# Optimization experiments

Measured on AMD Instinct MI355X. Metric: run time of the kernel, lower is better.

## Reference

```python
import jax, jax.numpy as jnp
import numpy as np

SLOPE = 0.01  # torch LeakyReLU default negative_slope

def _leaky(v):
    return jnp.where(v >= 0, v, SLOPE * v)

def _conv3d(x, w, b, stride):
    y = jax.lax.conv_general_dilated(
        x, w, window_strides=(stride, stride, stride), padding='VALID',
        dimension_numbers=('NCDHW', 'OIDHW', 'NCDHW'))
    return y + b[None, :, None, None, None]

def setup_inputs() -> dict:
    key = jax.random.key(0)
    ks = jax.random.split(key, 12)
    s = 0.05  # small init scale to keep exp(L1) numerically sane
    x = jax.random.normal(ks[0], (64, 1, 92, 92, 92), dtype=jnp.float32)
    w1 = jax.random.normal(ks[1], (16, 1, 6, 6, 6), dtype=jnp.float32) * s
    b1 = jnp.zeros((16,), jnp.float32)
    w2 = jax.random.normal(ks[2], (32, 16, 5, 5, 5), dtype=jnp.float32) * s
    b2 = jnp.zeros((32,), jnp.float32)
    w3 = jax.random.normal(ks[3], (48, 32, 5, 5, 5), dtype=jnp.float32) * s
    b3 = jnp.zeros((48,), jnp.float32)
    w4 = jax.random.normal(ks[4], (64, 48, 3, 3, 3), dtype=jnp.float32) * s
    b4 = jnp.zeros((64,), jnp.float32)
    T = jax.random.normal(ks[5], (512, 64 * 16), dtype=jnp.float32) * s
    Wm = jax.random.normal(ks[6], (512 + 64, 1), dtype=jnp.float32) * s
    bm = jnp.zeros((1,), jnp.float32)
    return {'x': x, 'w1': w1, 'b1': b1, 'w2': w2, 'b2': b2, 'w3': w3,
            'b3': b3, 'w4': w4, 'b4': b4, 'T': T, 'Wm': Wm, 'bm': bm}

def reference(x, w1, b1, w2, b2, w3, b3, w4, b4, T, Wm, bm):
    h = _leaky(_conv3d(x, w1, b1, 2))   # [N,16,44,44,44]
    h = _leaky(_conv3d(h, w2, b2, 3))   # [N,32,14,14,14]
    h = _leaky(_conv3d(h, w3, b3, 3))   # [N,48,4,4,4]
    h = _leaky(_conv3d(h, w4, b4, 1))   # [N,64,2,2,2]
    feature = h.reshape(h.shape[0], -1)  # [N,512]
    # minibatch discrimination: M [N,64,16]
    M = (feature @ T).reshape(-1, 64, 16)
    # pairwise L1 over last dim -> [N,N,64]; sum_j exp(.) -> [N,64]
    dist = jnp.sum(jnp.abs(M[:, None, :, :] - M[None, :, :, :]), axis=-1)
    out_T = jnp.sum(jnp.exp(dist), axis=1)
    z = jnp.concatenate([feature, out_T], axis=1) @ Wm + bm
    return jax.nn.sigmoid(z)
```

## Files before the change

### kernel.cpp

```cpp
#include <hip/hip_runtime.h>
#include <hip/hip_bf16.h>
#include <hip/hip_fp16.h>

typedef _Float16 v2h __attribute__((ext_vector_type(2)));
typedef _Float16 v8h __attribute__((ext_vector_type(8)));
typedef __fp16  v2hf __attribute__((ext_vector_type(2)));
typedef float v4f __attribute__((ext_vector_type(4)));

static inline __device__ float leaky(float v) { return v >= 0.f ? v : 0.01f * v; }

static inline __device__ v2h pkrtz(float a, float b) {
    v2hf r = __builtin_amdgcn_cvt_pkrtz(a, b);
    return __builtin_bit_cast(v2h, r);
}

#define W4T_OFF   0
#define H3P_OFF   82944
#define H3_OFF    1655808
#define FEAT_OFF  1852416
#define M_OFF     1885184
#define OT_OFF    1950720
#define F16_BASE  1954816
#define WL1_OFF   0
#define BF2_OFF   4608
#define BF3_OFF   81408
#define H2C_OFF   273408
#define H1C_OFF   5893120

__global__ void prep_kernel(const float* __restrict__ w1, const float* __restrict__ w2,
                            const float* __restrict__ w3, const float* __restrict__ w4,
                            float* __restrict__ w4t, _Float16* __restrict__ Bw1,
                            _Float16* __restrict__ Bf2, _Float16* __restrict__ Bf3) {
    int i = blockIdx.x * 256 + threadIdx.x;
    if (i < 4608) {
        int ks = i >> 9, l = (i >> 3) & 63, j = i & 7;
        int oc = l & 15, kg = l >> 4;
        int g = ks * 4 + kg;
        int kz = g / 6, ky = g % 6;
        Bw1[i] = (j < 6) ? (_Float16)w1[oc * 216 + kz * 36 + ky * 6 + j]
                         : (_Float16)0.f;
    } else if (i < 4608 + 76800) {
        int j2 = i - 4608;
        int nt = j2 / 38400, r = j2 % 38400;
        int t = r / 512, l = (r % 512) >> 3, j = r & 7;
        int oc = nt * 16 + (l & 15);
        int k = (l >> 4) * 8 + j;
        int kz = t / 15, ky = (t % 15) / 3, kxp = t % 3;
        int kx = kxp * 2 + (k >= 16 ? 1 : 0);
        int ic = k & 15;
        Bf2[j2] = (kx < 5) ? (_Float16)w2[oc * 2000 + ic * 125 + kz * 25 + ky * 5 + kx]
                           : (_Float16)0.f;
    } else if (i < 4608 + 76800 + 192000) {
        int j3 = i - (4608 + 76800);
        int nt = j3 / 64000, r = j3 % 64000;
        int tap = r / 512, l = (r % 512) >> 3, j = r & 7;
        int oc = nt * 16 + (l & 15);
        int ic = (l >> 4) * 8 + j;
        Bf3[j3] = (_Float16)w3[oc * 4000 + ic * 125 + tap];
    } else {
        int j4 = i - (4608 + 76800 + 192000);
        if (j4 < 82944) {
            int oc = j4 & 63, t = j4 >> 6;
            w4t[j4] = w4[oc * 1296 + t];
        }
    }
}

__global__ __launch_bounds__(256) void conv1_kernel(
    const float* __restrict__ x, const _Float16* __restrict__ Bw1,
    const float* __restrict__ b1, _Float16* __restrict__ h1c, int n0) {
    __shared__ __align__(16) _Float16 tile[144 * 96];
    int tid = threadIdx.x;
    int b = blockIdx.x;
    int nb = b / 121, rr = b % 121;
    int zq = rr / 11, yt = rr % 11;
    const float* xin = x + (long)(n0 + nb) * 778688;
    int izb = 8 * zq, iyb = 8 * yt;

    for (int u = tid; u < 3312; u += 256) {
        int row = u / 23, c = u % 23;
        int iz = izb + row / 12, iy = iyb + row % 12;
        const float4 v = *(const float4*)(xin + (long)iz * 8464 + iy * 92 + 4 * c);
        union { v2h h[2]; uint2 u2; } pk;
        pk.h[0] = pkrtz(v.x, v.y);
        pk.h[1] = pkrtz(v.z, v.w);
        *(uint2*)(tile + row * 96 + 4 * c) = pk.u2;
    }
    if (tid < 144) {
        uint2 zz; zz.x = 0u; zz.y = 0u;
        *(uint2*)(tile + tid * 96 + 92) = zz;
    }
    __syncthreads();

    int lane = tid & 63, wv = tid >> 6;
    int col = lane & 15, kg = lane >> 4;

    v8h Bv[9];
#pragma unroll
    for (int ks = 0; ks < 9; ks++) Bv[ks] = *(const v8h*)(Bw1 + ks * 512 + lane * 8);

    int offs[9];
#pragma unroll
    for (int ks = 0; ks < 9; ks++) {
        int g = ks * 4 + kg;
        int kz = g / 6, ky = g % 6;
        offs[ks] = (kz * 12 + ky) * 192;
    }
    float bias = b1[col];
    const uint* lds32 = (const uint*)tile;

    int z = zq * 4 + wv;
    for (int yy = 0; yy < 4; yy++) {
#pragma unroll
        for (int xt = 0; xt < 3; xt++) {
            int xo_base = (xt == 2) ? 28 : (xt << 4);
            int base_byte = (24 * wv + 2 * yy) * 192 + (xo_base + col) * 4;
            v4f acc = {0.f, 0.f, 0.f, 0.f};
#pragma unroll
            for (int ks = 0; ks < 9; ks++) {
                int di = (base_byte + offs[ks]) >> 2;
                union { uint u[4]; v8h h; } A;
                A.u[0] = lds32[di + 0];
                A.u[1] = lds32[di + 1];
                A.u[2] = lds32[di + 2];
                A.u[3] = lds32[di + 3];
                acc = __builtin_amdgcn_mfma_f32_16x16x32_f16(A.h, Bv[ks], acc, 0, 0, 0);
            }
            int y = yt * 4 + yy;
            long obase = ((long)((nb * 44 + z) * 44 + y) * 44 + xo_base + kg * 4) * 16 + col;
#pragma unroll
            for (int reg = 0; reg < 4; reg++) {
                h1c[obase + reg * 16] = (_Float16)leaky(acc[reg] + bias);
            }
        }
    }
}

__global__ __launch_bounds__(256) void conv2_kernel(
    const _Float16* __restrict__ h1c, const _Float16* __restrict__ Bf2,
    const float* __restrict__ b2, _Float16* __restrict__ h2c, int n0, int mlimit) {
    int tid = threadIdx.x;
    int lane = tid & 63, wv = tid >> 6;
    int t0 = (blockIdx.x * 4 + wv) * 2;
    int col = lane & 15, kgrp = lane >> 4;
    int par = kgrp >> 1, ico = (kgrp & 1) * 8;

    int base[2];
    bool valid[2];
#pragma unroll
    for (int i = 0; i < 2; i++) {
        int m = (t0 + i) * 16 + col;
        valid[i] = m < mlimit;
        int mm = valid[i] ? m : 0;
        int nl = mm / 2744, r = mm % 2744;
        int z = r / 196; r %= 196;
        int y = r / 14, xx = r % 14;
        base[i] = nl * 1362944 + z * 3 * 30976 + y * 3 * 704 + xx * 3 * 16 + ico + par * 16;
    }

    v4f acc[2][2];
#pragma unroll
    for (int i = 0; i < 2; i++)
#pragma unroll
        for (int nt = 0; nt < 2; nt++) acc[i][nt] = (v4f){0.f, 0.f, 0.f, 0.f};

    int t = 0;
    for (int kz = 0; kz < 5; kz++) {
        for (int ky = 0; ky < 5; ky++) {
#pragma unroll
            for (int kxp = 0; kxp < 3; kxp++, t++) {
                int d = kz * 30976 + ky * 704 + kxp * 32;
                v8h A0 = *(const v8h*)(h1c + base[0] + d);
                v8h A1 = *(const v8h*)(h1c + base[1] + d);
                v8h B0 = *(const v8h*)(Bf2 + t * 512 + lane * 8);
                v8h B1 = *(const v8h*)(Bf2 + (75 + t) * 512 + lane * 8);
                acc[0][0] = __builtin_amdgcn_mfma_f32_16x16x32_f16(A0, B0, acc[0][0], 0, 0, 0);
                acc[0][1] = __builtin_amdgcn_mfma_f32_16x16x32_f16(A0, B1, acc[0][1], 0, 0, 0);
                acc[1][0] = __builtin_amdgcn_mfma_f32_16x16x32_f16(A1, B0, acc[1][0], 0, 0, 0);
                acc[1][1] = __builtin_amdgcn_mfma_f32_16x16x32_f16(A1, B1, acc[1][1], 0, 0, 0);
            }
        }
    }

#pragma unroll
    for (int i = 0; i < 2; i++) {
        if (!valid[i]) continue;
#pragma unroll
        for (int nt = 0; nt < 2; nt++) {
            int oc = nt * 16 + col;
            float bb = b2[oc];
#pragma unroll
            for (int reg = 0; reg < 4; reg++) {
                int mlocal = (t0 + i) * 16 + kgrp * 4 + reg;
                float vv = leaky(acc[i][nt][reg] + bb);
                h2c[(long)(n0 * 2744 + mlocal) * 32 + oc] = (_Float16)vv;
            }
        }
    }
}

__global__ __launch_bounds__(256) void conv3_kernel(
    const _Float16* __restrict__ h2c, const _Float16* __restrict__ Bf3,
    float* __restrict__ h3p) {
    int tid = threadIdx.x;
    int lane = tid & 63, wv = tid >> 6;
    int mt = blockIdx.x * 4 + wv;
    int chunk = blockIdx.y;
    int col = lane & 15, kgrp = lane >> 4;
    int m = mt * 16 + col;
    int n = m >> 6, pos = m & 63;
    int z = pos >> 4, y = (pos >> 2) & 3, xx = pos & 3;
    int base = (n * 2744 + z * 3 * 196 + y * 3 * 14 + xx * 3) * 32 + kgrp * 8;

    v4f acc[3];
#pragma unroll
    for (int nt = 0; nt < 3; nt++) acc[nt] = (v4f){0.f, 0.f, 0.f, 0.f};

    int tap0 = chunk * 16;
    int tap1 = tap0 + 16 < 125 ? tap0 + 16 : 125;
    for (int tap = tap0; tap < tap1; tap++) {
        int kz = tap / 25, rr = tap % 25, ky = rr / 5, kx = rr % 5;
        int d = (kz * 196 + ky * 14 + kx) * 32;
        v8h A  = *(const v8h*)(h2c + base + d);
        v8h B0 = *(const v8h*)(Bf3 + tap * 512 + lane * 8);
        v8h B1 = *(const v8h*)(Bf3 + (125 + tap) * 512 + lane * 8);
        v8h B2 = *(const v8h*)(Bf3 + (250 + tap) * 512 + lane * 8);
        acc[0] = __builtin_amdgcn_mfma_f32_16x16x32_f16(A, B0, acc[0], 0, 0, 0);
        acc[1] = __builtin_amdgcn_mfma_f32_16x16x32_f16(A, B1, acc[1], 0, 0, 0);
        acc[2] = __builtin_amdgcn_mfma_f32_16x16x32_f16(A, B2, acc[2], 0, 0, 0);
    }

    float* outp = h3p + (long)chunk * 196608;
#pragma unroll
    for (int nt = 0; nt < 3; nt++)
#pragma unroll
        for (int reg = 0; reg < 4; reg++) {
            int md = mt * 16 + kgrp * 4 + reg;
            outp[md * 48 + nt * 16 + col] = acc[nt][reg];
        }
}

__global__ void combine3(float* __restrict__ h3, const float* __restrict__ h3p,
                         const float* __restrict__ b3) {
    int i = blockIdx.x * 256 + threadIdx.x;
    int m = i / 48, oc = i % 48;
    float v = b3[oc];
#pragma unroll
    for (int p = 0; p < 8; p++) v += h3p[i + p * 196608];
    h3[((m >> 6) * 48 + oc) * 64 + (m & 63)] = leaky(v);
}

__global__ void conv4_kernel(const float* __restrict__ h3, const float* __restrict__ w4t,
                             const float* __restrict__ b4, float* __restrict__ feat) {
    int o = blockIdx.x * 256 + threadIdx.x;
    int pos = o & 7;
    int oc  = (o >> 3) & 63;
    int n   = o >> 9;
    int px = pos & 1, py = (pos >> 1) & 1, pz = pos >> 2;
    const float* xn = h3 + (long)n * 48 * 64;
    float acc = 0.f;
    for (int ic = 0; ic < 48; ic++) {
        const float* xc = xn + ic * 64;
        int tb = ic * 27;
#pragma unroll
        for (int kz = 0; kz < 3; kz++)
#pragma unroll
            for (int ky = 0; ky < 3; ky++)
#pragma unroll
                for (int kx = 0; kx < 3; kx++) {
                    float v = xc[(pz + kz) * 16 + (py + ky) * 4 + (px + kx)];
                    acc += v * w4t[(tb + (kz * 3 + ky) * 3 + kx) * 64 + oc];
                }
    }
    feat[o] = leaky(acc + b4[oc]);
}

__global__ void m_kernel(const float* __restrict__ feat, const float* __restrict__ T,
                         float* __restrict__ M) {
    int o = blockIdx.x * 256 + threadIdx.x;
    int col = o & 1023;
    int n   = o >> 10;
    const float* fr = feat + n * 512;
    float acc = 0.f;
#pragma unroll 4
    for (int f = 0; f < 512; f++) acc += fr[f] * T[f * 1024 + col];
    M[o] = acc;
}

__global__ void outt_kernel(const float* __restrict__ M, float* __restrict__ oT) {
    int o = blockIdx.x * 256 + threadIdx.x;
    int k = o & 63;
    int i = o >> 6;
    float mi[16];
    const float4* Mi = (const float4*)(M + i * 1024 + k * 16);
#pragma unroll
    for (int q = 0; q < 4; q++) {
        float4 a = Mi[q];
        mi[q*4+0] = a.x; mi[q*4+1] = a.y; mi[q*4+2] = a.z; mi[q*4+3] = a.w;
    }
    float s = 0.f;
    for (int j = 0; j < 64; j++) {
        const float4* Mj = (const float4*)(M + j * 1024 + k * 16);
        float d = 0.f;
#pragma unroll
        for (int q = 0; q < 4; q++) {
            float4 a = Mj[q];
            d += fabsf(mi[q*4+0]-a.x) + fabsf(mi[q*4+1]-a.y) + fabsf(mi[q*4+2]-a.z) + fabsf(mi[q*4+3]-a.w);
        }
        s += __expf(d);
    }
    oT[o] = s;
}

__global__ void final_kernel(const float* __restrict__ feat, const float* __restrict__ oT,
                             const float* __restrict__ Wm, const float* __restrict__ bm,
                             float* __restrict__ out) {
    int i = blockIdx.x;
    int lane = threadIdx.x;
    const float* fr = feat + i * 512;
    float z = 0.f;
#pragma unroll
    for (int q = 0; q < 8; q++) z += fr[lane + q * 64] * Wm[lane + q * 64];
    z += oT[i * 64 + lane] * Wm[512 + lane];
#pragma unroll
    for (int off = 32; off > 0; off >>= 1) z += __shfl_down(z, off);
    if (lane == 0) out[i] = 1.f / (1.f + __expf(-(z + bm[0])));
}

extern "C" void kernel_launch(void* const* d_in, const int* in_sizes, int n_in,
                              void* d_out, int out_size, void* d_ws, size_t ws_size,
                              hipStream_t stream) {
    const float* x  = (const float*)d_in[0];
    const float* w1 = (const float*)d_in[1];
    const float* b1 = (const float*)d_in[2];
    const float* w2 = (const float*)d_in[3];
    const float* b2 = (const float*)d_in[4];
    const float* w3 = (const float*)d_in[5];
    const float* b3 = (const float*)d_in[6];
    const float* w4 = (const float*)d_in[7];
    const float* b4 = (const float*)d_in[8];
    const float* T  = (const float*)d_in[9];
    const float* Wm = (const float*)d_in[10];
    const float* bm = (const float*)d_in[11];

    float* ws   = (float*)d_ws;
    float* w4t  = ws + W4T_OFF;
    float* h3p  = ws + H3P_OFF;
    float* h3   = ws + H3_OFF;
    float* feat = ws + FEAT_OFF;
    float* Mb   = ws + M_OFF;
    float* oT   = ws + OT_OFF;
    _Float16* f16b = (_Float16*)(ws + F16_BASE);
    _Float16* Bw1  = f16b + WL1_OFF;
    _Float16* Bf2  = f16b + BF2_OFF;
    _Float16* Bf3  = f16b + BF3_OFF;
    _Float16* h2c  = f16b + H2C_OFF;
    _Float16* h1c  = f16b + H1C_OFF;

    prep_kernel<<<1392, 256, 0, stream>>>(w1, w2, w3, w4, w4t, Bw1, Bf2, Bf3);

    size_t fixed_bytes = (size_t)F16_BASE * 4 + (size_t)H1C_OFF * 2;
    int NB;
    if (ws_size >= fixed_bytes + (64ll * 1362944 + 64) * 2) NB = 64;
    else if (ws_size >= fixed_bytes + (16ll * 1362944 + 64) * 2) NB = 16;
    else NB = 8;

    for (int n0 = 0; n0 < 64; n0 += NB) {
        conv1_kernel<<<NB * 121, 256, 0, stream>>>(x, Bw1, b1, h1c, n0);
        int mlimit = NB * 2744;
        int blocks2 = (mlimit + 127) / 128;
        conv2_kernel<<<blocks2, 256, 0, stream>>>(h1c, Bf2, b2, h2c, n0, mlimit);
    }
    conv3_kernel<<<dim3(64, 8), 256, 0, stream>>>(h2c, Bf3, h3p);
    combine3<<<768, 256, 0, stream>>>(h3, h3p, b3);
    conv4_kernel<<<128, 256, 0, stream>>>(h3, w4t, b4, feat);
    m_kernel<<<256, 256, 0, stream>>>(feat, T, Mb);
    outt_kernel<<<16, 256, 0, stream>>>(Mb, oT);
    final_kernel<<<64, 64, 0, stream>>>(feat, oT, Wm, bm, (float*)d_out);
}
```

Before: 628.4 us.

## Enlarge conv2 tiles with XCD swizzle, fuse conv3 split-K reduction, rebalance tail kernels

conv2 now has each wave compute four M tiles instead of two, so every B-fragment load is reused by more MFMAs, and it remaps block IDs so consecutive tiles land on the same XCD. conv3 moves its split-K across the four waves of one block and reduces the partial sums in LDS, which removes the combine3 kernel and the partial-sum buffer round trip through global memory. conv4 uses smaller blocks for more parallelism, and outt splits the j loop across waves with an LDS reduction so 64 blocks can run. In exchange, conv2 needs more registers, which may lower occupancy, and conv3 has only 256 blocks, with one wave per block doing the final reduction.

```diff
diff --git a/kernel.cpp b/kernel.cpp
--- a/kernel.cpp
+++ b/kernel.cpp
@@ -141,26 +141,31 @@
     const float* __restrict__ b2, _Float16* __restrict__ h2c, int n0, int mlimit) {
     int tid = threadIdx.x;
     int lane = tid & 63, wv = tid >> 6;
-    int t0 = (blockIdx.x * 4 + wv) * 2;
+    int nwg = gridDim.x;
+    int orig = blockIdx.x;
+    int xcd = orig & 7, lid = orig >> 3;
+    int q = nwg >> 3, r = nwg & 7;
+    int swz = (xcd < r ? xcd * (q + 1) : r * (q + 1) + (xcd - r) * q) + lid;
+    int t0 = (swz * 4 + wv) * 4;
     int col = lane & 15, kgrp = lane >> 4;
     int par = kgrp >> 1, ico = (kgrp & 1) * 8;
 
-    int base[2];
-    bool valid[2];
-#pragma unroll
-    for (int i = 0; i < 2; i++) {
+    int base[4];
+    bool valid[4];
+#pragma unroll
+    for (int i = 0; i < 4; i++) {
         int m = (t0 + i) * 16 + col;
         valid[i] = m < mlimit;
         int mm = valid[i] ? m : 0;
-        int nl = mm / 2744, r = mm % 2744;
-        int z = r / 196; r %= 196;
-        int y = r / 14, xx = r % 14;
+        int nl = mm / 2744, rm = mm % 2744;
+        int z = rm / 196; rm %= 196;
+        int y = rm / 14, xx = rm % 14;
         base[i] = nl * 1362944 + z * 3 * 30976 + y * 3 * 704 + xx * 3 * 16 + ico + par * 16;
     }
 
-    v4f acc[2][2];
-#pragma unroll
-    for (int i = 0; i < 2; i++)
+    v4f acc[4][2];
+#pragma unroll
+    for (int i = 0; i < 4; i++)
 #pragma unroll
         for (int nt = 0; nt < 2; nt++) acc[i][nt] = (v4f){0.f, 0.f, 0.f, 0.f};
 
@@ -170,20 +175,26 @@
 #pragma unroll
             for (int kxp = 0; kxp < 3; kxp++, t++) {
                 int d = kz * 30976 + ky * 704 + kxp * 32;
+                v8h B0 = *(const v8h*)(Bf2 + t * 512 + lane * 8);
+                v8h B1 = *(const v8h*)(Bf2 + (75 + t) * 512 + lane * 8);
                 v8h A0 = *(const v8h*)(h1c + base[0] + d);
                 v8h A1 = *(const v8h*)(h1c + base[1] + d);
-                v8h B0 = *(const v8h*)(Bf2 + t * 512 + lane * 8);
-                v8h B1 = *(const v8h*)(Bf2 + (75 + t) * 512 + lane * 8);
+                v8h A2 = *(const v8h*)(h1c + base[2] + d);
+                v8h A3 = *(const v8h*)(h1c + base[3] + d);
                 acc[0][0] = __builtin_amdgcn_mfma_f32_16x16x32_f16(A0, B0, acc[0][0], 0, 0, 0);
                 acc[0][1] = __builtin_amdgcn_mfma_f32_16x16x32_f16(A0, B1, acc[0][1], 0, 0, 0);
                 acc[1][0] = __builtin_amdgcn_mfma_f32_16x16x32_f16(A1, B0, acc[1][0], 0, 0, 0);
                 acc[1][1] = __builtin_amdgcn_mfma_f32_16x16x32_f16(A1, B1, acc[1][1], 0, 0, 0);
+                acc[2][0] = __builtin_amdgcn_mfma_f32_16x16x32_f16(A2, B0, acc[2][0], 0, 0, 0);
+                acc[2][1] = __builtin_amdgcn_mfma_f32_16x16x32_f16(A2, B1, acc[2][1], 0, 0, 0);
+                acc[3][0] = __builtin_amdgcn_mfma_f32_16x16x32_f16(A3, B0, acc[3][0], 0, 0, 0);
+                acc[3][1] = __builtin_amdgcn_mfma_f32_16x16x32_f16(A3, B1, acc[3][1], 0, 0, 0);
             }
         }
     }
 
 #pragma unroll
-    for (int i = 0; i < 2; i++) {
+    for (int i = 0; i < 4; i++) {
         if (!valid[i]) continue;
 #pragma unroll
         for (int nt = 0; nt < 2; nt++) {
@@ -201,11 +212,11 @@
 
 __global__ __launch_bounds__(256) void conv3_kernel(
     const _Float16* __restrict__ h2c, const _Float16* __restrict__ Bf3,
-    float* __restrict__ h3p) {
+    const float* __restrict__ b3, float* __restrict__ h3) {
+    __shared__ float part[3][64][13];
     int tid = threadIdx.x;
     int lane = tid & 63, wv = tid >> 6;
-    int mt = blockIdx.x * 4 + wv;
-    int chunk = blockIdx.y;
+    int mt = blockIdx.x;
     int col = lane & 15, kgrp = lane >> 4;
     int m = mt * 16 + col;
     int n = m >> 6, pos = m & 63;
@@ -216,8 +227,8 @@
 #pragma unroll
     for (int nt = 0; nt < 3; nt++) acc[nt] = (v4f){0.f, 0.f, 0.f, 0.f};
 
-    int tap0 = chunk * 16;
-    int tap1 = tap0 + 16 < 125 ? tap0 + 16 : 125;
+    int tap0 = wv * 32;
+    int tap1 = tap0 + 32 < 125 ? tap0 + 32 : 125;
     for (int tap = tap0; tap < tap1; tap++) {
         int kz = tap / 25, rr = tap % 25, ky = rr / 5, kx = rr % 5;
         int d = (kz * 196 + ky * 14 + kx) * 32;
@@ -230,29 +241,38 @@
         acc[2] = __builtin_amdgcn_mfma_f32_16x16x32_f16(A, B2, acc[2], 0, 0, 0);
     }
 
-    float* outp = h3p + (long)chunk * 196608;
-#pragma unroll
-    for (int nt = 0; nt < 3; nt++)
-#pragma unroll
-        for (int reg = 0; reg < 4; reg++) {
-            int md = mt * 16 + kgrp * 4 + reg;
-            outp[md * 48 + nt * 16 + col] = acc[nt][reg];
-        }
-}
-
-__global__ void combine3(float* __restrict__ h3, const float* __restrict__ h3p,
-                         const float* __restrict__ b3) {
-    int i = blockIdx.x * 256 + threadIdx.x;
-    int m = i / 48, oc = i % 48;
-    float v = b3[oc];
-#pragma unroll
-    for (int p = 0; p < 8; p++) v += h3p[i + p * 196608];
-    h3[((m >> 6) * 48 + oc) * 64 + (m & 63)] = leaky(v);
+    if (wv > 0) {
+#pragma unroll
+        for (int nt = 0; nt < 3; nt++)
+#pragma unroll
+            for (int reg = 0; reg < 4; reg++)
+                part[wv - 1][lane][nt * 4 + reg] = acc[nt][reg];
+    }
+    __syncthreads();
+    if (wv == 0) {
+#pragma unroll
+        for (int w = 0; w < 3; w++)
+#pragma unroll
+            for (int nt = 0; nt < 3; nt++)
+#pragma unroll
+                for (int reg = 0; reg < 4; reg++)
+                    acc[nt][reg] += part[w][lane][nt * 4 + reg];
+#pragma unroll
+        for (int nt = 0; nt < 3; nt++) {
+            int oc = nt * 16 + col;
+            float bb = b3[oc];
+#pragma unroll
+            for (int reg = 0; reg < 4; reg++) {
+                int md = mt * 16 + kgrp * 4 + reg;
+                h3[((md >> 6) * 48 + oc) * 64 + (md & 63)] = leaky(acc[nt][reg] + bb);
+            }
+        }
+    }
 }
 
 __global__ void conv4_kernel(const float* __restrict__ h3, const float* __restrict__ w4t,
                              const float* __restrict__ b4, float* __restrict__ feat) {
-    int o = blockIdx.x * 256 + threadIdx.x;
+    int o = blockIdx.x * 128 + threadIdx.x;
     int pos = o & 7;
     int oc  = (o >> 3) & 63;
     int n   = o >> 9;
@@ -288,9 +308,10 @@
 }
 
 __global__ void outt_kernel(const float* __restrict__ M, float* __restrict__ oT) {
-    int o = blockIdx.x * 256 + threadIdx.x;
-    int k = o & 63;
-    int i = o >> 6;
+    __shared__ float part[3][64];
+    int i = blockIdx.x;
+    int tid = threadIdx.x;
+    int k = tid & 63, jq = tid >> 6;
     float mi[16];
     const float4* Mi = (const float4*)(M + i * 1024 + k * 16);
 #pragma unroll
@@ -299,7 +320,7 @@
         mi[q*4+0] = a.x; mi[q*4+1] = a.y; mi[q*4+2] = a.z; mi[q*4+3] = a.w;
     }
     float s = 0.f;
-    for (int j = 0; j < 64; j++) {
+    for (int j = jq * 16; j < jq * 16 + 16; j++) {
         const float4* Mj = (const float4*)(M + j * 1024 + k * 16);
         float d = 0.f;
 #pragma unroll
@@ -309,7 +330,12 @@
         }
         s += __expf(d);
     }
-    oT[o] = s;
+    if (jq > 0) part[jq - 1][k] = s;
+    __syncthreads();
+    if (jq == 0) {
+        s += part[0][k] + part[1][k] + part[2][k];
+        oT[i * 64 + k] = s;
+    }
 }
 
 __global__ void final_kernel(const float* __restrict__ feat, const float* __restrict__ oT,
@@ -345,7 +371,6 @@
 
     float* ws   = (float*)d_ws;
     float* w4t  = ws + W4T_OFF;
-    float* h3p  = ws + H3P_OFF;
     float* h3   = ws + H3_OFF;
     float* feat = ws + FEAT_OFF;
     float* Mb   = ws + M_OFF;
@@ -368,13 +393,12 @@
     for (int n0 = 0; n0 < 64; n0 += NB) {
         conv1_kernel<<<NB * 121, 256, 0, stream>>>(x, Bw1, b1, h1c, n0);
         int mlimit = NB * 2744;
-        int blocks2 = (mlimit + 127) / 128;
+        int blocks2 = (mlimit + 255) / 256;
         conv2_kernel<<<blocks2, 256, 0, stream>>>(h1c, Bf2, b2, h2c, n0, mlimit);
     }
-    conv3_kernel<<<dim3(64, 8), 256, 0, stream>>>(h2c, Bf3, h3p);
-    combine3<<<768, 256, 0, stream>>>(h3, h3p, b3);
-    conv4_kernel<<<128, 256, 0, stream>>>(h3, w4t, b4, feat);
+    conv3_kernel<<<256, 256, 0, stream>>>(h2c, Bf3, b3, h3);
+    conv4_kernel<<<256, 128, 0, stream>>>(h3, w4t, b4, feat);
     m_kernel<<<256, 256, 0, stream>>>(feat, T, Mb);
-    outt_kernel<<<16, 256, 0, stream>>>(Mb, oT);
+    outt_kernel<<<64, 256, 0, stream>>>(Mb, oT);
     final_kernel<<<64, 64, 0, stream>>>(feat, oT, Wm, bm, (float*)d_out);
 }
```

New measurement: 612.7 us. 1.03x faster.
